# Optimization experiments

Measured on AMD Instinct MI355X. Metric: run time of the kernel, lower is better.

## Reference

```python
import jax, jax.numpy as jnp
from jax import lax
import numpy as np

N_CLUSTERS = 8
G_CLUSTERS = 2
D_DIM = 512
DN = ('NCHW', 'OIHW', 'NCHW')


def _conv(x, w, b):
    y = lax.conv_general_dilated(x, w, window_strides=(1, 1), padding='VALID',
                                 dimension_numbers=DN)
    return y + b[None, :, None, None]


def setup_inputs() -> dict:
    key = jax.random.key(0)
    ks = jax.random.split(key, 6)
    B, D, H, W = 32, D_DIM, 7, 250
    KG = N_CLUSTERS + G_CLUSTERS
    scale = 1.0 / np.sqrt(D * 7)
    return {
        'x': jax.random.normal(ks[0], (B, D, H, W), dtype=jnp.float32),
        'feat_w': jax.random.normal(ks[1], (D, D, 7, 1), dtype=jnp.float32) * scale,
        'feat_b': jax.random.normal(ks[2], (D,), dtype=jnp.float32) * 0.01,
        'assign_w': jax.random.normal(ks[3], (KG, D, 7, 1), dtype=jnp.float32) * scale,
        'assign_b': jax.random.normal(ks[4], (KG,), dtype=jnp.float32) * 0.01,
        'centroids': jax.random.uniform(ks[5], (D, KG), dtype=jnp.float32),
    }


def reference(x, feat_w, feat_b, assign_w, assign_b, centroids):
    # features branch: conv(7,1) + ReLU -> (B, D, H', W)
    feat = jnp.maximum(_conv(x, feat_w, feat_b), 0.0)
    # assignment branch: conv(7,1) -> softmax over clusters -> (B, K+G, H', W)
    soft = jax.nn.softmax(_conv(x, assign_w, assign_b), axis=1)
    # Fused VLAD aggregation (mathematically identical to
    # sum_hw soft[b,k,hw] * (feat[b,d,hw] - centroids[d,k]) without
    # materializing the (B,D,K+G,H',W) residual tensor):
    s_sum = soft.sum(axis=(-2, -1))                                # (B, K+G)
    agg = jnp.einsum('bkhw,bdhw->bdk', soft, feat)                 # (B, D, K+G)
    cluster_res = agg - centroids[None, :, :] * s_sum[:, None, :]  # (B, D, K+G)
    cluster_res = cluster_res[..., :N_CLUSTERS]                    # drop ghost clusters
    # L2 normalize over feature dim (torch F.normalize, eps=1e-12)
    norm = jnp.sqrt(jnp.sum(cluster_res * cluster_res, axis=1, keepdims=True))
    cluster_l2 = cluster_res / jnp.maximum(norm, 1e-12)
    # (B, D, K) -> (B, K, D) -> (B, K*D)
    out = jnp.swapaxes(cluster_l2, 1, 2).reshape(x.shape[0], N_CLUSTERS * D_DIM)
    return out
```

## Files before the change

### kernel.cpp

```cpp
#include <hip/hip_runtime.h>
#include <stdint.h>

typedef float f32x4 __attribute__((ext_vector_type(4)));
typedef __bf16 bf16x8 __attribute__((ext_vector_type(8)));
typedef unsigned short ushortx8 __attribute__((ext_vector_type(8)));

#define D_DIM 512
#define KGC 10
#define NCLU 8
#define BATCH 32
#define WPOS 250
#define WPAD 256
#define KDIM 3584
#define MROWS 522
#define MPAD 528
#define MBIG 576
#define MHB 288
#define BN 128
#define KSPLIT 4
#define KCHUNK 896
#define NS 14
#define NT 64

__device__ __forceinline__ float bf2f(unsigned short u) {
  union { unsigned int i; float f; } v; v.i = ((unsigned int)u) << 16; return v.f;
}
__device__ __forceinline__ unsigned short f2bf(float f) {
  union { float f; unsigned int i; } v; v.f = f;
  unsigned int r = v.i + 0x7FFFu + ((v.i >> 16) & 1u);
  return (unsigned short)(r >> 16);
}

__device__ __forceinline__ void load_lds16(const void* g, void* l) {
  __builtin_amdgcn_global_load_lds(
      (const __attribute__((address_space(1))) void*)g,
      (__attribute__((address_space(3))) void*)l, 16, 0, 0);
}

__global__ void prep_kernel(const float* __restrict__ fw,
                            const float* __restrict__ fb,
                            const float* __restrict__ aw,
                            const float* __restrict__ ab,
                            unsigned short* __restrict__ Wcat,
                            float* __restrict__ bcat) {
  int r = blockIdx.x;
  unsigned short* dst = Wcat + (size_t)r * KDIM;
  const float* src = (r < D_DIM) ? (fw + (size_t)r * KDIM)
                   : (r < MROWS) ? (aw + (size_t)(r - D_DIM) * KDIM)
                                 : nullptr;
  for (int i = threadIdx.x; i < KDIM / 4; i += 256) {
    unsigned short o0 = 0, o1 = 0, o2 = 0, o3 = 0;
    if (src) {
      float4 v = ((const float4*)src)[i];
      o0 = f2bf(v.x); o1 = f2bf(v.y); o2 = f2bf(v.z); o3 = f2bf(v.w);
    }
    ushort4 o; o.x = o0; o.y = o1; o.z = o2; o.w = o3;
    ((ushort4*)dst)[i] = o;
  }
  if (threadIdx.x == 0)
    bcat[r] = r < D_DIM ? fb[r] : (r < MROWS ? ab[r - D_DIM] : 0.f);
}

__global__ __launch_bounds__(512, 4) void gemm_fused(
    const float* __restrict__ x, const unsigned short* __restrict__ Wcat,
    float* __restrict__ P) {
  __shared__ __align__(16) unsigned short Wl[MHB * 64];
  __shared__ __align__(16) unsigned short Xl[BN * 64];
  const int tid = threadIdx.x;
  const int nt = blockIdx.x, mh = blockIdx.y, sp = blockIdx.z;
  const int lane = tid & 63, wv = tid >> 6;
  const int wm = wv >> 2, wn = wv & 3;
  const int fr = lane & 15, kg = lane >> 4;
  const int sx = fr & 7;
  const int nloc = tid & 127, oc = tid >> 7;
  const int nglob = nt * BN + nloc;
  const int b = nglob >> 8, ncol = nglob & 255;
  const bool okn = ncol < WPOS;
  const float* xb = x + (size_t)b * KDIM * WPOS + ncol;
  const int kbase = sp * KCHUNK;
  const unsigned short* Wg = Wcat + (size_t)mh * MHB * KDIM + kbase;

  float xr[16];
  auto loadx = [&](int st) {
#pragma unroll
    for (int pass = 0; pass < 2; pass++) {
      int k0 = kbase + st * 64 + (oc + 4 * pass) * 8;
#pragma unroll
      for (int e = 0; e < 8; e++)
        xr[pass * 8 + e] = okn ? xb[(size_t)(k0 + e) * WPOS] : 0.f;
    }
  };

  f32x4 acc[9][2];
  const f32x4 zero = {0.f, 0.f, 0.f, 0.f};
#pragma unroll
  for (int f = 0; f < 9; f++) { acc[f][0] = zero; acc[f][1] = zero; }

  loadx(0);

  for (int st = 0; st < NS; st++) {
    __syncthreads();
#pragma unroll
    for (int it = 0; it < 5; it++) {
      int s = it * 512 + tid;
      if (s < MHB * 8) {
        int row = s >> 3, p = s & 7;
        int blk = p ^ (row & 7);
        load_lds16(Wg + (size_t)row * KDIM + st * 64 + blk * 8, &Wl[s * 8]);
      }
    }
#pragma unroll
    for (int pass = 0; pass < 2; pass++) {
      int oct = oc + 4 * pass;
      ushortx8 pk;
#pragma unroll
      for (int e = 0; e < 8; e++) pk[e] = f2bf(xr[pass * 8 + e]);
      *(ushortx8*)&Xl[nloc * 64 + (oct ^ (nloc & 7)) * 8] = pk;
    }
    __syncthreads();
    if (st + 1 < NS) loadx(st + 1);
#pragma unroll
    for (int ks = 0; ks < 2; ks++) {
      const int off = ((ks * 4 + kg) ^ sx) * 8;
      bf16x8 b0 = *(const bf16x8*)&Xl[(wn * 32 + fr) * 64 + off];
      bf16x8 b1 = *(const bf16x8*)&Xl[(wn * 32 + 16 + fr) * 64 + off];
#pragma unroll
      for (int f = 0; f < 9; f++) {
        bf16x8 af = *(const bf16x8*)&Wl[(wm * 144 + f * 16 + fr) * 64 + off];
        acc[f][0] = __builtin_amdgcn_mfma_f32_16x16x32_bf16(af, b0, acc[f][0], 0, 0, 0);
        acc[f][1] = __builtin_amdgcn_mfma_f32_16x16x32_bf16(af, b1, acc[f][1], 0, 0, 0);
      }
    }
  }

  float* Pb = P + (size_t)(((sp * 2 + mh) * NT) + nt) * (MHB * BN);
#pragma unroll
  for (int f = 0; f < 9; f++) {
    const int m = wm * 144 + f * 16 + kg * 4;
#pragma unroll
    for (int nf = 0; nf < 2; nf++) {
      const int n = wn * 32 + nf * 16 + fr;
#pragma unroll
      for (int r = 0; r < 4; r++)
        Pb[(size_t)(m + r) * BN + n] = acc[f][nf][r];
    }
  }
}

__global__ __launch_bounds__(256) void reduce_kernel(
    const float* __restrict__ P, const float* __restrict__ bcat,
    unsigned short* __restrict__ Y) {
  const int nt = blockIdx.x, mg = blockIdx.y;
  const int t = threadIdx.x;
  const int m = mg * 16 + (t >> 4);
  const int nl = (t & 15) * 8;
  if (m >= MPAD) return;
  const int mh = m >= MHB, ml = m - mh * MHB;
  const size_t slice = (size_t)MHB * BN;
  const size_t base = (size_t)ml * BN + nl;
  float s[8];
#pragma unroll
  for (int e = 0; e < 8; e++) s[e] = 0.f;
#pragma unroll
  for (int sp = 0; sp < KSPLIT; sp++) {
    const float* p = P + ((size_t)((sp * 2 + mh) * NT) + nt) * slice + base;
    float4 a = *(const float4*)p;
    float4 c = *(const float4*)(p + 4);
    s[0] += a.x; s[1] += a.y; s[2] += a.z; s[3] += a.w;
    s[4] += c.x; s[5] += c.y; s[6] += c.z; s[7] += c.w;
  }
  float bias = bcat[m];
  ushortx8 o;
#pragma unroll
  for (int e = 0; e < 8; e++) {
    float v = s[e] + bias;
    if (m < D_DIM) v = fmaxf(v, 0.f);
    o[e] = f2bf(v);
  }
  const int nglob = nt * BN + nl;
  const int bb = nglob >> 8, col = nglob & 255;
  *(ushortx8*)&Y[(size_t)bb * MPAD * WPAD + (size_t)m * WPAD + col] = o;
}

__global__ __launch_bounds__(512) void epi_kernel(
    const unsigned short* __restrict__ Y, const float* __restrict__ cent,
    float* __restrict__ out) {
  __shared__ float soft[WPAD];
  __shared__ float red[8];
  const int b = blockIdx.x >> 3, k = blockIdx.x & 7;
  const int tid = threadIdx.x;
  const unsigned short* Yb = Y + (size_t)b * MPAD * WPAD;

  float sv = 0.f;
  if (tid < WPOS) {
    float lg[KGC];
    float mx = -1e30f;
#pragma unroll
    for (int j = 0; j < KGC; j++) {
      lg[j] = bf2f(Yb[(size_t)(D_DIM + j) * WPAD + tid]);
      mx = fmaxf(mx, lg[j]);
    }
    float s = 0.f, ek = 0.f;
#pragma unroll
    for (int j = 0; j < KGC; j++) {
      float e = __expf(lg[j] - mx);
      s += e;
      if (j == k) ek = e;
    }
    sv = ek / s;
  }
  if (tid < WPAD) soft[tid] = sv;
  __syncthreads();

  float v = sv;
#pragma unroll
  for (int o = 32; o > 0; o >>= 1) v += __shfl_down(v, o, 64);
  if ((tid & 63) == 0) red[tid >> 6] = v;
  __syncthreads();
  float ssum = 0.f;
#pragma unroll
  for (int i = 0; i < 8; i++) ssum += red[i];

  float a[8];
#pragma unroll
  for (int u = 0; u < 8; u++) a[u] = 0.f;
  const unsigned short* row = Yb + (size_t)tid * WPAD;
  for (int w = 0; w < WPAD; w += 8) {
    ushortx8 f0 = *(const ushortx8*)(row + w);
    float4 s0 = *(const float4*)&soft[w];
    float4 s1 = *(const float4*)&soft[w + 4];
    a[0] += bf2f(f0[0]) * s0.x;
    a[1] += bf2f(f0[1]) * s0.y;
    a[2] += bf2f(f0[2]) * s0.z;
    a[3] += bf2f(f0[3]) * s0.w;
    a[4] += bf2f(f0[4]) * s1.x;
    a[5] += bf2f(f0[5]) * s1.y;
    a[6] += bf2f(f0[6]) * s1.z;
    a[7] += bf2f(f0[7]) * s1.w;
  }
  float asum = ((a[0] + a[1]) + (a[2] + a[3])) + ((a[4] + a[5]) + (a[6] + a[7]));
  float c = asum - cent[(size_t)tid * KGC + k] * ssum;

  __syncthreads();
  float q = c * c;
#pragma unroll
  for (int o = 32; o > 0; o >>= 1) q += __shfl_down(q, o, 64);
  if ((tid & 63) == 0) red[tid >> 6] = q;
  __syncthreads();
  float nsum = 0.f;
#pragma unroll
  for (int i = 0; i < 8; i++) nsum += red[i];
  float norm = sqrtf(nsum);
  float inv = 1.f / fmaxf(norm, 1e-12f);

  float* ob = out + (size_t)b * (NCLU * D_DIM) + (size_t)k * D_DIM;
  ob[tid] = c * inv;
}

extern "C" void kernel_launch(void* const* d_in, const int* in_sizes, int n_in,
                              void* d_out, int out_size, void* d_ws, size_t ws_size,
                              hipStream_t stream) {
  const float* x  = (const float*)d_in[0];
  const float* fw = (const float*)d_in[1];
  const float* fb = (const float*)d_in[2];
  const float* aw = (const float*)d_in[3];
  const float* ab = (const float*)d_in[4];
  const float* ce = (const float*)d_in[5];
  float* out = (float*)d_out;
  char* ws = (char*)d_ws;

  const size_t WC_BYTES = (size_t)MBIG * KDIM * 2;
  const size_t BC_BYTES = 4096;
  const size_t P_BYTES  = (size_t)KSPLIT * 2 * NT * MHB * BN * 4;
  unsigned short* Wc = (unsigned short*)(ws);
  float*          bc = (float*)(ws + WC_BYTES);
  float*          P  = (float*)(ws + WC_BYTES + BC_BYTES);
  unsigned short* Yv = (unsigned short*)(ws + WC_BYTES + BC_BYTES + P_BYTES);

  prep_kernel<<<MBIG, 256, 0, stream>>>(fw, fb, aw, ab, Wc, bc);
  gemm_fused<<<dim3(NT, 2, KSPLIT), 512, 0, stream>>>(x, Wc, P);
  reduce_kernel<<<dim3(NT, 36), 256, 0, stream>>>(P, bc, Yv);
  epi_kernel<<<BATCH * NCLU, 512, 0, stream>>>(Yv, ce, out);
}
```

Before: 245.8 us.

## Double-buffer LDS in GEMM and retile M into four 160-row blocks with split-K 2

The GEMM now double-buffers both the weight and activation tiles in LDS. Each step's async weight loads and x writes go to the next buffer while MFMAs run on the current one, and manual vmcnt/lgkmcnt waits need only one barrier per step. The M dimension is split into four 160-row blocks instead of two 288-row ones, and split-K drops from 4 to 2, so the grid stays at 512 blocks with fewer accumulators per thread. In exchange, x (which is read once per M block) is now read twice as often, and each block runs a longer K loop. The reduce kernel and the workspace layout are updated to match the new tiling.

Measured after the change: 251.5 us. 2.3% more time.

```diff
diff --git a/kernel.cpp b/kernel.cpp
--- a/kernel.cpp
+++ b/kernel.cpp
@@ -14,13 +14,18 @@
 #define KDIM 3584
 #define MROWS 522
 #define MPAD 528
-#define MBIG 576
-#define MHB 288
+#define MBIG 640
+#define BM 160
 #define BN 128
-#define KSPLIT 4
-#define KCHUNK 896
-#define NS 14
+#define KSPLIT 2
+#define KCHUNK 1792
+#define NS 28
 #define NT 64
+
+#define ASM_VMCNT16() asm volatile("s_waitcnt vmcnt(16)" ::: "memory")
+#define ASM_VMCNT0()  asm volatile("s_waitcnt vmcnt(0)" ::: "memory")
+#define ASM_LGKM0()   asm volatile("s_waitcnt lgkmcnt(0)" ::: "memory")
+#define BAR() do { __builtin_amdgcn_s_barrier(); __builtin_amdgcn_sched_barrier(0); } while (0)
 
 __device__ __forceinline__ float bf2f(unsigned short u) {
   union { unsigned int i; float f; } v; v.i = ((unsigned int)u) << 16; return v.f;
@@ -64,8 +69,8 @@
 __global__ __launch_bounds__(512, 4) void gemm_fused(
     const float* __restrict__ x, const unsigned short* __restrict__ Wcat,
     float* __restrict__ P) {
-  __shared__ __align__(16) unsigned short Wl[MHB * 64];
-  __shared__ __align__(16) unsigned short Xl[BN * 64];
+  __shared__ __align__(16) unsigned short Wl[2][BM * 64];
+  __shared__ __align__(16) unsigned short Xl[2][BN * 64];
   const int tid = threadIdx.x;
   const int nt = blockIdx.x, mh = blockIdx.y, sp = blockIdx.z;
   const int lane = tid & 63, wv = tid >> 6;
@@ -78,7 +83,7 @@
   const bool okn = ncol < WPOS;
   const float* xb = x + (size_t)b * KDIM * WPOS + ncol;
   const int kbase = sp * KCHUNK;
-  const unsigned short* Wg = Wcat + (size_t)mh * MHB * KDIM + kbase;
+  const unsigned short* Wg = Wcat + (size_t)mh * BM * KDIM + kbase;
 
   float xr[16];
   auto loadx = [&](int st) {
@@ -90,53 +95,71 @@
         xr[pass * 8 + e] = okn ? xb[(size_t)(k0 + e) * WPOS] : 0.f;
     }
   };
-
-  f32x4 acc[9][2];
-  const f32x4 zero = {0.f, 0.f, 0.f, 0.f};
-#pragma unroll
-  for (int f = 0; f < 9; f++) { acc[f][0] = zero; acc[f][1] = zero; }
-
-  loadx(0);
-
-  for (int st = 0; st < NS; st++) {
-    __syncthreads();
-#pragma unroll
-    for (int it = 0; it < 5; it++) {
-      int s = it * 512 + tid;
-      if (s < MHB * 8) {
-        int row = s >> 3, p = s & 7;
-        int blk = p ^ (row & 7);
-        load_lds16(Wg + (size_t)row * KDIM + st * 64 + blk * 8, &Wl[s * 8]);
-      }
-    }
+  auto stageW = [&](int st, int buf) {
+#pragma unroll
+    for (int it = 0; it < 3; it++) {
+      int s = (it < 2) ? it * 512 + tid : 1024 + (tid & 255);
+      int row = s >> 3, p = s & 7;
+      int blk = p ^ (row & 7);
+      load_lds16(Wg + (size_t)row * KDIM + st * 64 + blk * 8, &Wl[buf][s * 8]);
+    }
+  };
+  auto writeX = [&](int buf) {
 #pragma unroll
     for (int pass = 0; pass < 2; pass++) {
       int oct = oc + 4 * pass;
       ushortx8 pk;
 #pragma unroll
       for (int e = 0; e < 8; e++) pk[e] = f2bf(xr[pass * 8 + e]);
-      *(ushortx8*)&Xl[nloc * 64 + (oct ^ (nloc & 7)) * 8] = pk;
-    }
-    __syncthreads();
-    if (st + 1 < NS) loadx(st + 1);
+      *(ushortx8*)&Xl[buf][nloc * 64 + (oct ^ (nloc & 7)) * 8] = pk;
+    }
+  };
+
+  f32x4 acc[5][2];
+  const f32x4 zero = {0.f, 0.f, 0.f, 0.f};
+#pragma unroll
+  for (int f = 0; f < 5; f++) { acc[f][0] = zero; acc[f][1] = zero; }
+
+  loadx(0);
+  stageW(0, 0);
+  writeX(0);
+  loadx(1);
+  ASM_VMCNT16();
+  ASM_LGKM0();
+  BAR();
+
+  for (int t = 0; t < NS; ++t) {
+    const int cur = t & 1, nxt = cur ^ 1;
+    const bool more = (t + 1 < NS);
+    if (more) {
+      stageW(t + 1, nxt);
+      writeX(nxt);
+    }
+    if (t + 2 < NS) loadx(t + 2);
 #pragma unroll
     for (int ks = 0; ks < 2; ks++) {
       const int off = ((ks * 4 + kg) ^ sx) * 8;
-      bf16x8 b0 = *(const bf16x8*)&Xl[(wn * 32 + fr) * 64 + off];
-      bf16x8 b1 = *(const bf16x8*)&Xl[(wn * 32 + 16 + fr) * 64 + off];
-#pragma unroll
-      for (int f = 0; f < 9; f++) {
-        bf16x8 af = *(const bf16x8*)&Wl[(wm * 144 + f * 16 + fr) * 64 + off];
+      bf16x8 b0 = *(const bf16x8*)&Xl[cur][(wn * 32 + fr) * 64 + off];
+      bf16x8 b1 = *(const bf16x8*)&Xl[cur][(wn * 32 + 16 + fr) * 64 + off];
+#pragma unroll
+      for (int f = 0; f < 5; f++) {
+        bf16x8 af = *(const bf16x8*)&Wl[cur][(wm * 80 + f * 16 + fr) * 64 + off];
         acc[f][0] = __builtin_amdgcn_mfma_f32_16x16x32_bf16(af, b0, acc[f][0], 0, 0, 0);
         acc[f][1] = __builtin_amdgcn_mfma_f32_16x16x32_bf16(af, b1, acc[f][1], 0, 0, 0);
       }
     }
-  }
-
-  float* Pb = P + (size_t)(((sp * 2 + mh) * NT) + nt) * (MHB * BN);
-#pragma unroll
-  for (int f = 0; f < 9; f++) {
-    const int m = wm * 144 + f * 16 + kg * 4;
+    if (more) {
+      if (t + 2 < NS) { ASM_VMCNT16(); }
+      else            { ASM_VMCNT0();  }
+      ASM_LGKM0();
+      BAR();
+    }
+  }
+
+  float* Pb = P + (size_t)((sp * 4 + mh) * NT + nt) * (BM * BN);
+#pragma unroll
+  for (int f = 0; f < 5; f++) {
+    const int m = wm * 80 + f * 16 + kg * 4;
 #pragma unroll
     for (int nf = 0; nf < 2; nf++) {
       const int n = wn * 32 + nf * 16 + fr;
@@ -155,15 +178,16 @@
   const int m = mg * 16 + (t >> 4);
   const int nl = (t & 15) * 8;
   if (m >= MPAD) return;
-  const int mh = m >= MHB, ml = m - mh * MHB;
-  const size_t slice = (size_t)MHB * BN;
+  const int mh = (m >= 480) ? 3 : (m >= 320) ? 2 : (m >= 160) ? 1 : 0;
+  const int ml = m - mh * BM;
+  const size_t slice = (size_t)BM * BN;
   const size_t base = (size_t)ml * BN + nl;
   float s[8];
 #pragma unroll
   for (int e = 0; e < 8; e++) s[e] = 0.f;
 #pragma unroll
   for (int sp = 0; sp < KSPLIT; sp++) {
-    const float* p = P + ((size_t)((sp * 2 + mh) * NT) + nt) * slice + base;
+    const float* p = P + ((size_t)((sp * 4 + mh) * NT) + nt) * slice + base;
     float4 a = *(const float4*)p;
     float4 c = *(const float4*)(p + 4);
     s[0] += a.x; s[1] += a.y; s[2] += a.z; s[3] += a.w;
@@ -271,14 +295,14 @@
 
   const size_t WC_BYTES = (size_t)MBIG * KDIM * 2;
   const size_t BC_BYTES = 4096;
-  const size_t P_BYTES  = (size_t)KSPLIT * 2 * NT * MHB * BN * 4;
+  const size_t P_BYTES  = (size_t)KSPLIT * 4 * NT * BM * BN * 4;
   unsigned short* Wc = (unsigned short*)(ws);
   float*          bc = (float*)(ws + WC_BYTES);
   float*          P  = (float*)(ws + WC_BYTES + BC_BYTES);
   unsigned short* Yv = (unsigned short*)(ws + WC_BYTES + BC_BYTES + P_BYTES);
 
   prep_kernel<<<MBIG, 256, 0, stream>>>(fw, fb, aw, ab, Wc, bc);
-  gemm_fused<<<dim3(NT, 2, KSPLIT), 512, 0, stream>>>(x, Wc, P);
-  reduce_kernel<<<dim3(NT, 36), 256, 0, stream>>>(P, bc, Yv);
+  gemm_fused<<<dim3(NT, 4, KSPLIT), 512, 0, stream>>>(x, Wc, P);
+  reduce_kernel<<<dim3(NT, 40), 256, 0, stream>>>(P, bc, Yv);
   epi_kernel<<<BATCH * NCLU, 512, 0, stream>>>(Yv, ce, out);
 }
```
